# Kernel tuning notes

Hardware: AMD Instinct MI355X
Metric: run time of the kernel (lower is better)

## Reference

```python
import jax, jax.numpy as jnp
import numpy as np

B, N, C = 128, 197, 768
H = 12
HID = 3072
DROP = 0.1
EPS = 1e-5


def _layernorm(x, g, b):
    m = jnp.mean(x, axis=-1, keepdims=True)
    v = jnp.var(x, axis=-1, keepdims=True)
    return (x - m) * jax.lax.rsqrt(v + EPS) * g + b


def setup_inputs() -> dict:
    key = jax.random.key(0)
    ks = jax.random.split(key, 6)
    def lin(k, fan_in, fan_out):
        return (jax.random.normal(k, (fan_in, fan_out), jnp.float32) * (fan_in ** -0.5))
    return {
        "x": jax.random.normal(ks[0], (B, N, C), jnp.float32),
        "ln1_g": jnp.ones((C,), jnp.float32),
        "ln1_b": jnp.zeros((C,), jnp.float32),
        "Wqkv": lin(ks[1], C, 3 * C),          # qkv_bias=False
        "Wproj": lin(ks[2], C, C),
        "bproj": jnp.zeros((C,), jnp.float32),
        "ln2_g": jnp.ones((C,), jnp.float32),
        "ln2_b": jnp.zeros((C,), jnp.float32),
        "W1": lin(ks[3], C, HID),
        "b1": jnp.zeros((HID,), jnp.float32),
        "W2": lin(ks[4], HID, C),
        "b2": jnp.zeros((C,), jnp.float32),
    }


def reference(x, ln1_g, ln1_b, Wqkv, Wproj, bproj, ln2_g, ln2_b, W1, b1, W2, b2):
    Bx, Nx, Cx = x.shape
    hd = Cx // H
    thr = int((Nx - 1) * DROP)            # 19
    keep = (Nx - 1) - (thr + 1)           # 176 patches kept (rank > thr)

    # ---- drop_low_attn: unscaled q@k^T, mean over heads, cls->patch scores ----
    qkv = (x @ Wqkv).reshape(Bx, Nx, 3, H, hd).transpose(2, 0, 3, 1, 4)
    q, k = qkv[0], qkv[1]
    attn0 = jnp.einsum('bhnd,bhmd->bhnm', q, k)        # no scale, no softmax
    scores = jnp.mean(attn0, axis=1)[:, 0, 1:]          # [B, N-1]
    rank = jnp.argsort(jnp.argsort(scores, axis=1), axis=1)
    keep_mask = rank > thr                              # exactly `keep` True per row
    # indices of kept patches in original order (stable argsort of ~mask)
    idx = jnp.argsort((~keep_mask).astype(jnp.int32), axis=1)[:, :keep] + 1
    tok = jnp.concatenate([jnp.zeros((Bx, 1), idx.dtype), idx], axis=1)  # cls + kept
    x = jnp.take_along_axis(x, tok[:, :, None], axis=1) / (1.0 - DROP)   # [B, 177, C]
    Np = keep + 1

    # ---- attention block (scaled softmax attention) ----
    h = _layernorm(x, ln1_g, ln1_b)
    qkv2 = (h @ Wqkv).reshape(Bx, Np, 3, H, hd).transpose(2, 0, 3, 1, 4)
    q2, k2, v2 = qkv2[0], qkv2[1], qkv2[2]
    a = jax.nn.softmax(jnp.einsum('bhnd,bhmd->bhnm', q2, k2) * (hd ** -0.5), axis=-1)
    o = jnp.einsum('bhnm,bhmd->bhnd', a, v2).transpose(0, 2, 1, 3).reshape(Bx, Np, Cx)
    x = x + (o @ Wproj + bproj)

    # ---- MLP block ----
    h = _layernorm(x, ln2_g, ln2_b)
    x = x + (jax.nn.gelu(h @ W1 + b1, approximate=False) @ W2 + b2)
    return x
```

## Files before the change

### kernel.cpp

```cpp
#include <hip/hip_runtime.h>
#include <math.h>

#define BB 128
#define NTOK 197
#define CC 768
#define HH 12
#define HD 64
#define HIDN 3072
#define NP 177
#define NPATCH 196
#define THRK 19
#define MR (BB*NP)

using short8 = __attribute__((ext_vector_type(8))) short;
using f32x4  = __attribute__((ext_vector_type(4))) float;

__device__ __forceinline__ unsigned short f2b(float f){
  unsigned u = __builtin_bit_cast(unsigned, f);
  u += 0x7fffu + ((u >> 16) & 1u);
  return (unsigned short)(u >> 16);
}

__device__ __forceinline__ float b2f(unsigned short s){
  unsigned u = (unsigned)s << 16;
  return __builtin_bit_cast(float, u);
}

__device__ __forceinline__ float fast_gelu(float v){
  float u = v * 0.70710678118654752f;
  float a = fabsf(u);
  float t = 1.0f / fmaf(0.3275911f, a, 1.0f);
  float p = fmaf(1.061405429f, t, -1.453152027f);
  p = fmaf(p, t, 1.421413741f);
  p = fmaf(p, t, -0.284496736f);
  p = fmaf(p, t, 0.254829592f);
  p = p * t;
  float e = __expf(-a*a);
  float erfu = copysignf(1.0f - p*e, u);
  return 0.5f * v * (1.0f + erfu);
}

__device__ __forceinline__ void gload16(const void* src, void* lds){
  __builtin_amdgcn_global_load_lds(
      (const __attribute__((address_space(1))) unsigned int*)src,
      (__attribute__((address_space(3))) unsigned int*)lds,
      16, 0, 0);
}

__global__ void tcvt_kernel(const float* __restrict__ in, unsigned short* __restrict__ out, int K, int N){
  __shared__ float tile[64][65];
  int n0 = blockIdx.x*64, k0 = blockIdx.y*64;
  int t = threadIdx.x;
  int r = t >> 6, c = t & 63;
  #pragma unroll
  for (int i = 0; i < 16; ++i)
    tile[r + i*4][c] = in[(size_t)(k0 + r + i*4)*N + n0 + c];
  __syncthreads();
  #pragma unroll
  for (int i = 0; i < 16; ++i)
    out[(size_t)(n0 + r + i*4)*K + k0 + c] = f2b(tile[c][r + i*4]);
}

__global__ void q0_kernel(const float* __restrict__ x, const float* __restrict__ Wqkv, float* __restrict__ q0){
  int b = blockIdx.x, t = threadIdx.x;
  int c = blockIdx.y*256 + t;
  __shared__ float xs[CC];
  for (int j = t; j < CC; j += 256) xs[j] = x[(size_t)b*NTOK*CC + j];
  __syncthreads();
  double acc = 0.0;
  for (int j = 0; j < CC; ++j) acc = fma((double)xs[j], (double)Wqkv[(size_t)j*(3*CC) + c], acc);
  q0[b*CC + c] = (float)acc;
}

__global__ void wvec_kernel(const float* __restrict__ Wqkv, const float* __restrict__ q0, float* __restrict__ wv){
  int b = blockIdx.x;
  int j = blockIdx.y*4 + (threadIdx.x >> 6);
  int l = threadIdx.x & 63;
  const float* row = Wqkv + (size_t)j*(3*CC) + CC;
  const float* qs = q0 + b*CC;
  double acc = 0.0;
  for (int c = l; c < CC; c += 64) acc = fma((double)row[c], (double)qs[c], acc);
  for (int off = 32; off; off >>= 1) acc += __shfl_down(acc, off);
  if (l == 0) wv[b*CC + j] = (float)acc;
}

__global__ void score_kernel(const float* __restrict__ x, const float* __restrict__ wv, float* __restrict__ sc){
  int m = blockIdx.x, b = blockIdx.y, l = threadIdx.x;
  const float* xr = x + ((size_t)b*NTOK + 1 + m)*CC;
  const float* wr = wv + b*CC;
  double acc = 0.0;
  for (int c = l; c < CC; c += 64) acc = fma((double)xr[c], (double)wr[c], acc);
  for (int off = 32; off; off >>= 1) acc += __shfl_down(acc, off);
  if (l == 0) sc[b*NPATCH + m] = (float)(acc * (1.0/12.0));
}

__global__ void select_kernel(const float* __restrict__ sc, int* __restrict__ tok){
  int b = blockIdx.x, t = threadIdx.x;
  __shared__ float s[NPATCH];
  __shared__ int kp[NPATCH];
  for (int m = t; m < NPATCH; m += 256) s[m] = sc[b*NPATCH + m];
  __syncthreads();
  for (int m = t; m < NPATCH; m += 256){
    float v = s[m]; int rank = 0;
    for (int j = 0; j < NPATCH; ++j){
      float u = s[j];
      rank += (u < v) || (u == v && j < m);
    }
    kp[m] = (rank > THRK) ? 1 : 0;
  }
  __syncthreads();
  for (int m = t; m < NPATCH; m += 256){
    if (kp[m]){
      int pos = 0;
      for (int j = 0; j < m; ++j) pos += kp[j];
      tok[b*NP + 1 + pos] = m + 1;
    }
  }
  if (t == 0) tok[b*NP] = 0;
}

__global__ void gln_kernel(const float* __restrict__ x, const int* __restrict__ tok,
                           const float* __restrict__ g, const float* __restrict__ bt,
                           unsigned short* __restrict__ xkb, unsigned short* __restrict__ hout){
  int row = blockIdx.x, t = threadIdx.x;
  int b = row / NP;
  int src = tok[row];
  const float* xr = x + ((size_t)b*NTOK + src)*CC;
  float v0 = xr[t]*(1.0f/0.9f), v1 = xr[t+256]*(1.0f/0.9f), v2 = xr[t+512]*(1.0f/0.9f);
  float s = v0+v1+v2, ss = v0*v0+v1*v1+v2*v2;
  for (int off = 32; off; off >>= 1){ s += __shfl_down(s, off); ss += __shfl_down(ss, off); }
  __shared__ float red[8];
  int wid = t >> 6, lane = t & 63;
  if (lane == 0){ red[wid] = s; red[4+wid] = ss; }
  __syncthreads();
  if (t == 0){
    float S = red[0]+red[1]+red[2]+red[3], SS = red[4]+red[5]+red[6]+red[7];
    float mean = S * (1.0f/CC);
    float var = SS * (1.0f/CC) - mean*mean;
    red[0] = mean; red[1] = rsqrtf(var + 1e-5f);
  }
  __syncthreads();
  float mean = red[0], rstd = red[1];
  unsigned short* xrow = xkb + (size_t)row*CC;
  unsigned short* orow = hout + (size_t)row*CC;
  xrow[t]     = f2b(v0); xrow[t+256] = f2b(v1); xrow[t+512] = f2b(v2);
  orow[t]     = f2b((v0-mean)*rstd*g[t]     + bt[t]);
  orow[t+256] = f2b((v1-mean)*rstd*g[t+256] + bt[t+256]);
  orow[t+512] = f2b((v2-mean)*rstd*g[t+512] + bt[t+512]);
}

__global__ void ln_kernel(const float* __restrict__ in, const float* __restrict__ g,
                          const float* __restrict__ bt, unsigned short* __restrict__ out){
  int row = blockIdx.x, t = threadIdx.x;
  const float* xr = in + (size_t)row*CC;
  float v0 = xr[t], v1 = xr[t+256], v2 = xr[t+512];
  float s = v0+v1+v2, ss = v0*v0+v1*v1+v2*v2;
  for (int off = 32; off; off >>= 1){ s += __shfl_down(s, off); ss += __shfl_down(ss, off); }
  __shared__ float red[8];
  int wid = t >> 6, lane = t & 63;
  if (lane == 0){ red[wid] = s; red[4+wid] = ss; }
  __syncthreads();
  if (t == 0){
    float S = red[0]+red[1]+red[2]+red[3], SS = red[4]+red[5]+red[6]+red[7];
    float mean = S * (1.0f/CC);
    float var = SS * (1.0f/CC) - mean*mean;
    red[0] = mean; red[1] = rsqrtf(var + 1e-5f);
  }
  __syncthreads();
  float mean = red[0], rstd = red[1];
  unsigned short* orow = out + (size_t)row*CC;
  orow[t]     = f2b((v0-mean)*rstd*g[t]     + bt[t]);
  orow[t+256] = f2b((v1-mean)*rstd*g[t+256] + bt[t+256]);
  orow[t+512] = f2b((v2-mean)*rstd*g[t+512] + bt[t+512]);
}

template<int EPI>
__global__ __launch_bounds__(256, 3) void gemm128(
    const unsigned short* __restrict__ A, const unsigned short* __restrict__ Bt,
    const float* __restrict__ bias, const void* __restrict__ res, void* __restrict__ outp,
    int M, int N, int K)
{
  __shared__ __align__(16) short lds[3*8192];
  int nwg = gridDim.x, o = blockIdx.x;
  int q = nwg >> 3, rr = nwg & 7;
  int xcd = o & 7, seq = o >> 3;
  int wg = (xcd < rr) ? xcd*(q+1) + seq : rr*(q+1) + (xcd - rr)*q + seq;
  int nx = N >> 7;
  int m0 = (wg / nx) << 7, n0 = (wg % nx) << 7;

  int t = threadIdx.x, w = t >> 6, l = t & 63;
  int wr = w >> 1, wc = w & 1;
  f32x4 acc[4][4] = {};
  int nt = K >> 5;

  auto stage = [&](int kti, int sb){
    int kt = kti << 5;
    short* buf = &lds[sb*8192];
    #pragma unroll
    for (int j = 0; j < 2; ++j){
      int row = j*64 + w*16 + (l >> 2);
      int gk = ((l & 3) ^ ((row >> 1) & 3)) * 8;
      gload16(A  + (size_t)(m0 + row)*K + kt + gk, &buf[(j*64 + w*16)*32]);
      gload16(Bt + (size_t)(n0 + row)*K + kt + gk, &buf[4096 + (j*64 + w*16)*32]);
    }
  };
  auto compute = [&](int cb){
    const short* Ab = &lds[cb*8192];
    const short* Bb = Ab + 4096;
    short8 af[4], bf[4];
    #pragma unroll
    for (int i = 0; i < 4; ++i){
      int Ra = wr*64 + i*16 + (l & 15);
      af[i] = *reinterpret_cast<const short8*>(&Ab[Ra*32 + (((l>>4) ^ ((Ra>>1)&3)))*8]);
      int Rb = wc*64 + i*16 + (l & 15);
      bf[i] = *reinterpret_cast<const short8*>(&Bb[Rb*32 + (((l>>4) ^ ((Rb>>1)&3)))*8]);
    }
    __builtin_amdgcn_s_setprio(1);
    #pragma unroll
    for (int i = 0; i < 4; ++i)
      #pragma unroll
      for (int jn = 0; jn < 4; ++jn)
        acc[i][jn] = __builtin_amdgcn_mfma_f32_16x16x32_bf16(af[i], bf[jn], acc[i][jn], 0, 0, 0);
    __builtin_amdgcn_s_setprio(0);
  };
  auto step = [&](int ti, int cb, int sb){
    bool more = (ti + 2) < nt;
    if (more) stage(ti + 2, sb);
    compute(cb);
    if (more) asm volatile("s_waitcnt vmcnt(4)" ::: "memory");
    else      asm volatile("s_waitcnt vmcnt(0)" ::: "memory");
    __builtin_amdgcn_s_barrier();
    asm volatile("" ::: "memory");
  };

  stage(0, 0); stage(1, 1);
  asm volatile("s_waitcnt vmcnt(4)" ::: "memory");
  __builtin_amdgcn_s_barrier();
  asm volatile("" ::: "memory");

  #pragma unroll 1
  for (int ti = 0; ti < nt; ti += 3){
    step(ti,     0, 2);
    step(ti + 1, 1, 0);
    step(ti + 2, 2, 1);
  }

  #pragma unroll
  for (int i = 0; i < 4; ++i)
  #pragma unroll
  for (int jn = 0; jn < 4; ++jn){
    int row = m0 + wr*64 + i*16 + (l>>4)*4;
    int col = n0 + wc*64 + jn*16 + (l&15);
    #pragma unroll
    for (int r = 0; r < 4; ++r){
      float v = acc[i][jn][r];
      if (EPI != 0) v += bias[col];
      if (EPI == 2) v = fast_gelu(v);
      if (EPI == 1) v += b2f(((const unsigned short*)res)[(size_t)(row+r)*N + col]);
      if (EPI == 3) v += ((const float*)res)[(size_t)(row+r)*N + col];
      if (EPI == 0 || EPI == 2) ((unsigned short*)outp)[(size_t)(row+r)*N + col] = f2b(v);
      else                      ((float*)outp)[(size_t)(row+r)*N + col] = v;
    }
  }
}

__global__ __launch_bounds__(256) void attn_kernel(const unsigned short* __restrict__ qkv2,
                                                   unsigned short* __restrict__ o)
{
  int rt = blockIdx.x, h = blockIdx.y, b = blockIdx.z;
  int t = threadIdx.x, w = t >> 6, l = t & 63;
  __shared__ short Vt[64*192];
  __shared__ short P[4][16*192];
  for (int idx = t; idx < NP*8; idx += 256){
    int m = idx >> 3, d0 = (idx & 7)*8;
    short8 v = *reinterpret_cast<const short8*>(qkv2 + (size_t)(b*NP+m)*(3*CC) + 2*CC + h*HD + d0);
    #pragma unroll
    for (int j = 0; j < 8; ++j) Vt[(d0+j)*192 + m] = v[j];
  }
  for (int idx = t; idx < 64*15; idx += 256){
    int d = idx/15, m = NP + idx%15;
    Vt[d*192 + m] = 0;
  }
  __syncthreads();
  int nb = rt*64 + w*16;
  int g = l >> 4, c = l & 15;
  int nq = nb + c; if (nq > NP-1) nq = NP-1;
  const unsigned short* qrow = qkv2 + (size_t)(b*NP+nq)*(3*CC) + h*HD + 8*g;
  short8 aq0 = *reinterpret_cast<const short8*>(qrow);
  short8 aq1 = *reinterpret_cast<const short8*>(qrow + 32);
  f32x4 acc[12];
  #pragma unroll
  for (int ct = 0; ct < 12; ++ct){
    int m = ct*16 + c; if (m > NP-1) m = NP-1;
    const unsigned short* krow = qkv2 + (size_t)(b*NP+m)*(3*CC) + CC + h*HD + 8*g;
    short8 bk0 = *reinterpret_cast<const short8*>(krow);
    short8 bk1 = *reinterpret_cast<const short8*>(krow + 32);
    f32x4 a = {};
    a = __builtin_amdgcn_mfma_f32_16x16x32_bf16(aq0, bk0, a, 0, 0, 0);
    a = __builtin_amdgcn_mfma_f32_16x16x32_bf16(aq1, bk1, a, 0, 0, 0);
    acc[ct] = a;
  }
  float mx[4] = {-INFINITY, -INFINITY, -INFINITY, -INFINITY};
  #pragma unroll
  for (int ct = 0; ct < 12; ++ct){
    bool valid = (ct*16 + c) < NP;
    #pragma unroll
    for (int r = 0; r < 4; ++r){
      float v = valid ? acc[ct][r]*0.125f : -INFINITY;
      acc[ct][r] = v;
      mx[r] = fmaxf(mx[r], v);
    }
  }
  #pragma unroll
  for (int off = 1; off < 16; off <<= 1){
    #pragma unroll
    for (int r = 0; r < 4; ++r) mx[r] = fmaxf(mx[r], __shfl_xor(mx[r], off));
  }
  float sm2[4] = {0.f, 0.f, 0.f, 0.f};
  #pragma unroll
  for (int ct = 0; ct < 12; ++ct)
    #pragma unroll
    for (int r = 0; r < 4; ++r){
      float e = __expf(acc[ct][r] - mx[r]);
      acc[ct][r] = e; sm2[r] += e;
    }
  #pragma unroll
  for (int off = 1; off < 16; off <<= 1){
    #pragma unroll
    for (int r = 0; r < 4; ++r) sm2[r] += __shfl_xor(sm2[r], off);
  }
  float inv[4];
  #pragma unroll
  for (int r = 0; r < 4; ++r) inv[r] = 1.0f / sm2[r];
  #pragma unroll
  for (int ct = 0; ct < 12; ++ct)
    #pragma unroll
    for (int r = 0; r < 4; ++r)
      P[w][(4*g + r)*192 + ct*16 + c] = (short)f2b(acc[ct][r]*inv[r]);
  f32x4 acc2[4] = {};
  __builtin_amdgcn_s_setprio(1);
  #pragma unroll
  for (int ks = 0; ks < 6; ++ks){
    short8 pa = *reinterpret_cast<const short8*>(&P[w][c*192 + ks*32 + 8*g]);
    #pragma unroll
    for (int ct2 = 0; ct2 < 4; ++ct2){
      short8 bv = *reinterpret_cast<const short8*>(&Vt[(ct2*16 + c)*192 + ks*32 + 8*g]);
      acc2[ct2] = __builtin_amdgcn_mfma_f32_16x16x32_bf16(pa, bv, acc2[ct2], 0, 0, 0);
    }
  }
  __builtin_amdgcn_s_setprio(0);
  #pragma unroll
  for (int ct2 = 0; ct2 < 4; ++ct2){
    #pragma unroll
    for (int r = 0; r < 4; ++r){
      int n = nb + 4*g + r;
      if (n < NP) o[(size_t)(b*NP+n)*CC + h*HD + ct2*16 + c] = f2b(acc2[ct2][r]);
    }
  }
}

extern "C" void kernel_launch(void* const* d_in, const int* in_sizes, int n_in,
                              void* d_out, int out_size, void* d_ws, size_t ws_size,
                              hipStream_t stream) {
  const float* x     = (const float*)d_in[0];
  const float* ln1g  = (const float*)d_in[1];
  const float* ln1b  = (const float*)d_in[2];
  const float* Wqkv  = (const float*)d_in[3];
  const float* Wproj = (const float*)d_in[4];
  const float* bproj = (const float*)d_in[5];
  const float* ln2g  = (const float*)d_in[6];
  const float* ln2b  = (const float*)d_in[7];
  const float* W1    = (const float*)d_in[8];
  const float* b1    = (const float*)d_in[9];
  const float* W2    = (const float*)d_in[10];
  const float* b2    = (const float*)d_in[11];
  float* out = (float*)d_out;

  unsigned char* base = (unsigned char*)d_ws;
  size_t off = 0;
  auto alloc = [&](size_t bytes) -> void* {
    off = (off + 255) & ~(size_t)255;
    void* p = base + off;
    off += bytes;
    return p;
  };
  unsigned short* WqkvT  = (unsigned short*)alloc((size_t)(3*CC)*CC*2);
  unsigned short* WprojT = (unsigned short*)alloc((size_t)CC*CC*2);
  unsigned short* W1T    = (unsigned short*)alloc((size_t)HIDN*CC*2);
  unsigned short* W2T    = (unsigned short*)alloc((size_t)CC*HIDN*2);
  float* q0   = (float*)alloc((size_t)BB*CC*4);
  float* wv   = (float*)alloc((size_t)BB*CC*4);
  float* sc   = (float*)alloc((size_t)BB*NPATCH*4);
  int*   tok  = (int*)alloc((size_t)BB*NP*4);
  unsigned short* hbuf = (unsigned short*)alloc((size_t)MR*CC*2);
  unsigned short* xkb  = (unsigned short*)alloc((size_t)MR*CC*2);
  unsigned short* qkv2 = (unsigned short*)alloc((size_t)MR*3*CC*2);
  if (off > ws_size) return;

  unsigned short* obuf = hbuf;
  unsigned short* mid  = xkb;
  float* x2 = out;

  tcvt_kernel<<<dim3((3*CC)/64, CC/64), 256, 0, stream>>>(Wqkv,  WqkvT,  CC, 3*CC);
  tcvt_kernel<<<dim3(CC/64, CC/64),     256, 0, stream>>>(Wproj, WprojT, CC, CC);
  tcvt_kernel<<<dim3(HIDN/64, CC/64),   256, 0, stream>>>(W1,    W1T,    CC, HIDN);
  tcvt_kernel<<<dim3(CC/64, HIDN/64),   256, 0, stream>>>(W2,    W2T,    HIDN, CC);

  q0_kernel<<<dim3(BB, 3), 256, 0, stream>>>(x, Wqkv, q0);
  wvec_kernel<<<dim3(BB, CC/4), 256, 0, stream>>>(Wqkv, q0, wv);
  score_kernel<<<dim3(NPATCH, BB), 64, 0, stream>>>(x, wv, sc);
  select_kernel<<<BB, 256, 0, stream>>>(sc, tok);

  gln_kernel<<<MR, 256, 0, stream>>>(x, tok, ln1g, ln1b, xkb, hbuf);

  gemm128<0><<<(MR/128)*((3*CC)/128), 256, 0, stream>>>(hbuf, WqkvT, nullptr, nullptr, qkv2, MR, 3*CC, CC);
  attn_kernel<<<dim3(3, HH, BB), 256, 0, stream>>>(qkv2, obuf);
  gemm128<1><<<(MR/128)*(CC/128), 256, 0, stream>>>(obuf, WprojT, bproj, xkb, x2, MR, CC, CC);

  ln_kernel<<<MR, 256, 0, stream>>>(x2, ln2g, ln2b, hbuf);
  gemm128<2><<<(MR/128)*(HIDN/128), 256, 0, stream>>>(hbuf, W1T, b1, nullptr, mid, MR, HIDN, CC);
  gemm128<3><<<(MR/128)*(CC/128), 256, 0, stream>>>(mid, W2T, b2, x2, out, MR, CC, HIDN);
}
```

Baseline: 752.5 us.

## Enlarge GEMM tiles to 256x256 with 512 threads and padded M

```diff
diff --git a/kernel.cpp b/kernel.cpp
--- a/kernel.cpp
+++ b/kernel.cpp
@@ -11,6 +11,7 @@
 #define NPATCH 196
 #define THRK 19
 #define MR (BB*NP)
+#define MRP 22784
 
 using short8 = __attribute__((ext_vector_type(8))) short;
 using f32x4  = __attribute__((ext_vector_type(4))) float;
@@ -175,58 +176,79 @@
 }
 
 template<int EPI>
-__global__ __launch_bounds__(256, 3) void gemm128(
+__global__ __launch_bounds__(512, 2) void gemm256(
     const unsigned short* __restrict__ A, const unsigned short* __restrict__ Bt,
     const float* __restrict__ bias, const void* __restrict__ res, void* __restrict__ outp,
-    int M, int N, int K)
+    int Mreal, int N, int K)
 {
-  __shared__ __align__(16) short lds[3*8192];
+  __shared__ __align__(16) short lds[3*16384];
   int nwg = gridDim.x, o = blockIdx.x;
   int q = nwg >> 3, rr = nwg & 7;
   int xcd = o & 7, seq = o >> 3;
   int wg = (xcd < rr) ? xcd*(q+1) + seq : rr*(q+1) + (xcd - rr)*q + seq;
-  int nx = N >> 7;
-  int m0 = (wg / nx) << 7, n0 = (wg % nx) << 7;
+  int nx = N >> 8;
+  int m0 = (wg / nx) << 8, n0 = (wg % nx) << 8;
 
   int t = threadIdx.x, w = t >> 6, l = t & 63;
-  int wr = w >> 1, wc = w & 1;
-  f32x4 acc[4][4] = {};
+  int wr = w >> 2, wc = w & 3;
+  f32x4 acc[8][4] = {};
   int nt = K >> 5;
 
   auto stage = [&](int kti, int sb){
     int kt = kti << 5;
-    short* buf = &lds[sb*8192];
-    #pragma unroll
-    for (int j = 0; j < 2; ++j){
-      int row = j*64 + w*16 + (l >> 2);
-      int gk = ((l & 3) ^ ((row >> 1) & 3)) * 8;
-      gload16(A  + (size_t)(m0 + row)*K + kt + gk, &buf[(j*64 + w*16)*32]);
-      gload16(Bt + (size_t)(n0 + row)*K + kt + gk, &buf[4096 + (j*64 + w*16)*32]);
-    }
-  };
-  auto compute = [&](int cb){
-    const short* Ab = &lds[cb*8192];
-    const short* Bb = Ab + 4096;
-    short8 af[4], bf[4];
-    #pragma unroll
-    for (int i = 0; i < 4; ++i){
-      int Ra = wr*64 + i*16 + (l & 15);
-      af[i] = *reinterpret_cast<const short8*>(&Ab[Ra*32 + (((l>>4) ^ ((Ra>>1)&3)))*8]);
-      int Rb = wc*64 + i*16 + (l & 15);
-      bf[i] = *reinterpret_cast<const short8*>(&Bb[Rb*32 + (((l>>4) ^ ((Rb>>1)&3)))*8]);
-    }
+    short* buf = &lds[sb*16384];
+    #pragma unroll
+    for (int i = 0; i < 2; ++i){
+      int idx = i*512 + t;
+      int row = idx >> 2, c = idx & 3;
+      int cg = c ^ ((row >> 1) & 3);
+      gload16(A + (size_t)(m0 + row)*K + kt + cg*8, &buf[idx*8]);
+    }
+    #pragma unroll
+    for (int i = 0; i < 2; ++i){
+      int idx = i*512 + t;
+      int row = idx >> 2, c = idx & 3;
+      int cg = c ^ ((row >> 1) & 3);
+      gload16(Bt + (size_t)(n0 + row)*K + kt + cg*8, &buf[8192 + idx*8]);
+    }
+  };
+  auto readB = [&](int cb, short8* bfr){
+    const short* Bb = &lds[cb*16384 + 8192];
+    #pragma unroll
+    for (int j = 0; j < 4; ++j){
+      int row = wc*64 + j*16 + (l & 15);
+      int ck = (l >> 4) ^ ((row >> 1) & 3);
+      bfr[j] = *reinterpret_cast<const short8*>(&Bb[row*32 + ck*8]);
+    }
+  };
+  auto readA2 = [&](int cb, int qd, short8* afr){
+    const short* Ab = &lds[cb*16384];
+    #pragma unroll
+    for (int f = 0; f < 2; ++f){
+      int row = wr*128 + qd*32 + f*16 + (l & 15);
+      int ck = (l >> 4) ^ ((row >> 1) & 3);
+      afr[f] = *reinterpret_cast<const short8*>(&Ab[row*32 + ck*8]);
+    }
+  };
+  auto mfma8 = [&](const short8* afr, const short8* bfr, int qd){
     __builtin_amdgcn_s_setprio(1);
     #pragma unroll
-    for (int i = 0; i < 4; ++i)
+    for (int f = 0; f < 2; ++f)
       #pragma unroll
-      for (int jn = 0; jn < 4; ++jn)
-        acc[i][jn] = __builtin_amdgcn_mfma_f32_16x16x32_bf16(af[i], bf[jn], acc[i][jn], 0, 0, 0);
+      for (int j = 0; j < 4; ++j)
+        acc[qd*2+f][j] = __builtin_amdgcn_mfma_f32_16x16x32_bf16(afr[f], bfr[j], acc[qd*2+f][j], 0, 0, 0);
     __builtin_amdgcn_s_setprio(0);
   };
   auto step = [&](int ti, int cb, int sb){
     bool more = (ti + 2) < nt;
     if (more) stage(ti + 2, sb);
-    compute(cb);
+    short8 bfr[4], af0[2], af1[2];
+    readB(cb, bfr);
+    readA2(cb, 0, af0);
+    readA2(cb, 1, af1);  mfma8(af0, bfr, 0);
+    readA2(cb, 2, af0);  mfma8(af1, bfr, 1);
+    readA2(cb, 3, af1);  mfma8(af0, bfr, 2);
+                         mfma8(af1, bfr, 3);
     if (more) asm volatile("s_waitcnt vmcnt(4)" ::: "memory");
     else      asm volatile("s_waitcnt vmcnt(0)" ::: "memory");
     __builtin_amdgcn_s_barrier();
@@ -246,20 +268,25 @@
   }
 
   #pragma unroll
-  for (int i = 0; i < 4; ++i)
-  #pragma unroll
-  for (int jn = 0; jn < 4; ++jn){
-    int row = m0 + wr*64 + i*16 + (l>>4)*4;
-    int col = n0 + wc*64 + jn*16 + (l&15);
-    #pragma unroll
-    for (int r = 0; r < 4; ++r){
-      float v = acc[i][jn][r];
-      if (EPI != 0) v += bias[col];
-      if (EPI == 2) v = fast_gelu(v);
-      if (EPI == 1) v += b2f(((const unsigned short*)res)[(size_t)(row+r)*N + col]);
-      if (EPI == 3) v += ((const float*)res)[(size_t)(row+r)*N + col];
-      if (EPI == 0 || EPI == 2) ((unsigned short*)outp)[(size_t)(row+r)*N + col] = f2b(v);
-      else                      ((float*)outp)[(size_t)(row+r)*N + col] = v;
+  for (int rf = 0; rf < 8; ++rf){
+    int row0 = m0 + wr*128 + rf*16 + (l >> 4)*4;
+    #pragma unroll
+    for (int j = 0; j < 4; ++j){
+      int col = n0 + wc*64 + j*16 + (l & 15);
+      #pragma unroll
+      for (int r = 0; r < 4; ++r){
+        int row = row0 + r;
+        float v = acc[rf][j][r];
+        if (EPI != 0) v += bias[col];
+        if (EPI == 2) v = fast_gelu(v);
+        if (EPI == 0 || EPI == 2){
+          ((unsigned short*)outp)[(size_t)row*N + col] = f2b(v);
+        } else if (row < Mreal){
+          if (EPI == 1) v += b2f(((const unsigned short*)res)[(size_t)row*N + col]);
+          else          v += ((const float*)res)[(size_t)row*N + col];
+          ((float*)outp)[(size_t)row*N + col] = v;
+        }
+      }
     }
   }
 }
@@ -392,14 +419,16 @@
   float* wv   = (float*)alloc((size_t)BB*CC*4);
   float* sc   = (float*)alloc((size_t)BB*NPATCH*4);
   int*   tok  = (int*)alloc((size_t)BB*NP*4);
-  unsigned short* hbuf = (unsigned short*)alloc((size_t)MR*CC*2);
-  unsigned short* xkb  = (unsigned short*)alloc((size_t)MR*CC*2);
-  unsigned short* qkv2 = (unsigned short*)alloc((size_t)MR*3*CC*2);
+  unsigned short* hbuf = (unsigned short*)alloc((size_t)MRP*CC*2);
+  unsigned short* xkb  = (unsigned short*)alloc((size_t)MRP*CC*2);
+  unsigned short* qkv2 = (unsigned short*)alloc((size_t)MRP*3*CC*2);
   if (off > ws_size) return;
 
   unsigned short* obuf = hbuf;
   unsigned short* mid  = xkb;
   float* x2 = out;
+
+  hipMemsetAsync(hbuf + (size_t)MR*CC, 0, (size_t)(MRP-MR)*CC*2, stream);
 
   tcvt_kernel<<<dim3((3*CC)/64, CC/64), 256, 0, stream>>>(Wqkv,  WqkvT,  CC, 3*CC);
   tcvt_kernel<<<dim3(CC/64, CC/64),     256, 0, stream>>>(Wproj, WprojT, CC, CC);
@@ -413,11 +442,11 @@
 
   gln_kernel<<<MR, 256, 0, stream>>>(x, tok, ln1g, ln1b, xkb, hbuf);
 
-  gemm128<0><<<(MR/128)*((3*CC)/128), 256, 0, stream>>>(hbuf, WqkvT, nullptr, nullptr, qkv2, MR, 3*CC, CC);
+  gemm256<0><<<(MRP/256)*((3*CC)/256), 512, 0, stream>>>(hbuf, WqkvT, nullptr, nullptr, qkv2, MR, 3*CC, CC);
   attn_kernel<<<dim3(3, HH, BB), 256, 0, stream>>>(qkv2, obuf);
-  gemm128<1><<<(MR/128)*(CC/128), 256, 0, stream>>>(obuf, WprojT, bproj, xkb, x2, MR, CC, CC);
+  gemm256<1><<<(MRP/256)*(CC/256), 512, 0, stream>>>(obuf, WprojT, bproj, xkb, x2, MR, CC, CC);
 
   ln_kernel<<<MR, 256, 0, stream>>>(x2, ln2g, ln2b, hbuf);
-  gemm128<2><<<(MR/128)*(HIDN/128), 256, 0, stream>>>(hbuf, W1T, b1, nullptr, mid, MR, HIDN, CC);
-  gemm128<3><<<(MR/128)*(CC/128), 256, 0, stream>>>(mid, W2T, b2, x2, out, MR, CC, HIDN);
-}
+  gemm256<2><<<(MRP/256)*(HIDN/256), 512, 0, stream>>>(hbuf, W1T, b1, nullptr, mid, MR, HIDN, CC);
+  gemm256<3><<<(MRP/256)*(CC/256), 512, 0, stream>>>(mid, W2T, b2, x2, out, MR, CC, HIDN);
+}
```

Result: slower. 902.7 us (+20.0%).
